# Optimization experiments

Hardware: AMD Instinct MI355X
Metric: run time of the kernel (lower is better)

## Reference

```python
import jax, jax.numpy as jnp
import numpy as np

T, B, D = 512, 16, 128   # cur_seq, batch, d_input
H = 8                    # n_heads
DH = D                   # d_head_inner = d_input in TemporalTX
P = 512                  # prev_seq = hgcn_rollout_len


def setup_inputs() -> dict:
    key = jax.random.key(0)
    ks = jax.random.split(key, 8)
    inp = {
        "inputs": jax.random.normal(ks[0], (T, B, D), jnp.float32),
        "memory": jax.random.normal(ks[1], (2, P, B, D), jnp.float32),  # n_layers+1 = 2
        "w_kv": jax.random.normal(ks[2], (2 * H * DH, D), jnp.float32) * 0.02,
        "w_q": jax.random.normal(ks[3], (H * DH, D), jnp.float32) * 0.02,
        "w_p": jax.random.normal(ks[4], (H * DH, D), jnp.float32) * 0.02,
        "w_out": jax.random.normal(ks[5], (D, H * DH), jnp.float32) * 0.02,
        "u": jax.random.normal(ks[6], (H, DH), jnp.float32) * 0.02,
        "v": jax.random.normal(ks[7], (H, DH), jnp.float32) * 0.02,
    }
    return inp


def _rel_shift(x):
    # x: [I, J, B, H] -> Transformer-XL relative shift
    I, J, b, h = x.shape
    zp = jnp.zeros((I, 1, b, h), x.dtype)
    return jnp.concatenate([zp, x], axis=1).reshape(J + 1, I, b, h)[1:].reshape(I, J, b, h)


def _pos_embs(J, d):
    # positions counting down: J-1 ... 0
    pos = jnp.arange(J - 1, -1, -1, dtype=jnp.float32)
    inv_freq = 1.0 / (10000.0 ** (jnp.arange(0.0, d, 2.0) / d))
    sin_inp = pos[:, None] * inv_freq[None, :]          # [J, d/2]
    return jnp.concatenate([jnp.sin(sin_inp), jnp.cos(sin_inp)], axis=-1)  # [J, d]


def _attention(x, mem, pe, w_kv, w_q, w_p, w_out, u, v, mask):
    cs, bs, _ = x.shape
    J = cs + mem.shape[0]
    xm = jnp.concatenate([mem, x], axis=0)              # [J, B, D]
    kv = jnp.einsum('jbe,fe->jbf', xm, w_kv)            # [J, B, 2*H*DH]
    k, vv = jnp.split(kv, 2, axis=-1)
    k = k.reshape(J, bs, H, DH)
    vv = vv.reshape(J, bs, H, DH)
    q = jnp.einsum('ibe,fe->ibf', x, w_q).reshape(cs, bs, H, DH)
    content = jnp.einsum('ibhd,jbhd->ijbh', q + u, k)   # [I, J, B, H]
    p = jnp.einsum('je,fe->jf', pe, w_p).reshape(J, H, DH)
    position = jnp.einsum('ibhd,jhd->ijbh', q + v, p)
    position = _rel_shift(position)
    attn = content + position
    attn = jnp.where(mask[:, :, None, None], -jnp.inf, attn)
    scale = 1.0 / (DH ** 0.5)
    attn = jax.nn.softmax(attn * scale, axis=1)
    out = jnp.einsum('ijbh,jbhd->ibhd', attn, vv).reshape(cs, bs, H * DH)
    return jnp.einsum('ibf,ef->ibe', out, w_out)        # [I, B, D]


def reference(inputs, memory, w_kv, w_q, w_p, w_out, u, v):
    cs, bs = inputs.shape[:2]
    mem = list(memory)                                   # unbind along layer dim
    ps = mem[0].shape[0]
    J = cs + ps
    mask = jnp.triu(jnp.ones((cs, J), bool), k=1 + ps)   # [cs, J]
    pe = _pos_embs(J, D)                                 # [J, D]
    layer_out = _attention(inputs, mem[0], pe, w_kv, w_q, w_p, w_out, u, v, mask)
    hidden = [inputs, layer_out]
    # update_memory: keep last ps entries of cat(mem, hidden), detached
    new_mem = []
    end = ps + cs
    beg = max(0, end - ps)
    for m, h in zip(mem, hidden):
        cat = jnp.concatenate([m, h], axis=0)
        new_mem.append(jax.lax.stop_gradient(cat[beg:end]))
    return layer_out, jnp.stack(new_mem)
```

## Files before the change

### kernel.cpp

```cpp
#include <hip/hip_runtime.h>


typedef short s16x8 __attribute__((ext_vector_type(8)));
typedef float f32x4 __attribute__((ext_vector_type(4)));

#define MFMA(a, b, c) __builtin_amdgcn_mfma_f32_16x16x32_bf16((a), (b), (c), 0, 0, 0)
#define LDS_FENCE() asm volatile("s_waitcnt lgkmcnt(0)" ::: "memory")

__device__ __forceinline__ unsigned short f2b(float f) {
  unsigned int x = __builtin_bit_cast(unsigned int, f);
  x += 0x7fffu + ((x >> 16) & 1u);
  return (unsigned short)(x >> 16);
}
__device__ __forceinline__ s16x8 ldg8(const unsigned short* p) {
  return *(const s16x8*)p;
}
__device__ __forceinline__ s16x8 ldf8(const float* p) {
  float4 u = ((const float4*)p)[0];
  float4 v = ((const float4*)p)[1];
  s16x8 r;
  r[0] = (short)f2b(u.x); r[1] = (short)f2b(u.y);
  r[2] = (short)f2b(u.z); r[3] = (short)f2b(u.w);
  r[4] = (short)f2b(v.x); r[5] = (short)f2b(v.y);
  r[6] = (short)f2b(v.z); r[7] = (short)f2b(v.w);
  return r;
}
__device__ __forceinline__ void gl2lds(const unsigned short* g, unsigned short* l) {
  __builtin_amdgcn_global_load_lds(
      (const __attribute__((address_space(1))) unsigned int*)(g),
      (__attribute__((address_space(3))) unsigned int*)(l), 16, 0, 0);
}

__global__ __launch_bounds__(256, 2) void k_prep(
    const float* __restrict__ wkv, const float* __restrict__ wq,
    const float* __restrict__ wp, const float* __restrict__ wout,
    unsigned short* __restrict__ wkv_b, unsigned short* __restrict__ wq_b,
    unsigned short* __restrict__ wp_b, unsigned short* __restrict__ wout_b) {
  int id = blockIdx.x * 256 + threadIdx.x;
  const float* src;
  unsigned short* dst;
  int off;
  if (id < 32768) { src = wkv; dst = wkv_b; off = id; }
  else if (id < 49152) { src = wq; dst = wq_b; off = id - 32768; }
  else if (id < 65536) { src = wp; dst = wp_b; off = id - 49152; }
  else { src = wout; dst = wout_b; off = id - 65536; }
  ((s16x8*)dst)[off] = ldf8(src + off * 8);
}

__global__ __launch_bounds__(256, 2) void k_proj(
    const float* __restrict__ x, const float* __restrict__ mem,
    const unsigned short* __restrict__ wkv_b, const unsigned short* __restrict__ wp_b,
    unsigned short* __restrict__ Kk, unsigned short* __restrict__ Vt,
    unsigned short* __restrict__ Pp) {
  __shared__ float tbuf[4][16][128];
  const int lane = threadIdx.x & 63;
  const int w = threadIdx.x >> 6;
  const int l15 = lane & 15, l4 = lane >> 4;

  if (blockIdx.x < 1024) {
    const int ncg = (blockIdx.x & 7) * 2;
    const int b = (blockIdx.x >> 3) & 15;
    const int jb = (blockIdx.x >> 7) * 128 + w * 32;

    s16x8 A[2][4];
#pragma unroll
    for (int g = 0; g < 2; ++g) {
      int jr = jb + g * 16 + l15;
      const float* arow =
          (jr < 512 ? mem + (jr * 16 + b) * 128 : x + ((jr - 512) * 16 + b) * 128) + l4 * 8;
      A[g][0] = ldf8(arow); A[g][1] = ldf8(arow + 32);
      A[g][2] = ldf8(arow + 64); A[g][3] = ldf8(arow + 96);
    }

    for (int q = 0; q < 2; ++q) {
      const int nc = ncg + q;
      f32x4 acc[2][8] = {};
#pragma unroll
      for (int fc = 0; fc < 8; ++fc) {
        const unsigned short* brow = wkv_b + (nc * 128 + fc * 16 + l15) * 128 + l4 * 8;
        s16x8 b0 = ldg8(brow), b1 = ldg8(brow + 32), b2 = ldg8(brow + 64), b3 = ldg8(brow + 96);
#pragma unroll
        for (int g = 0; g < 2; ++g) {
          acc[g][fc] = MFMA(A[g][0], b0, acc[g][fc]);
          acc[g][fc] = MFMA(A[g][1], b1, acc[g][fc]);
          acc[g][fc] = MFMA(A[g][2], b2, acc[g][fc]);
          acc[g][fc] = MFMA(A[g][3], b3, acc[g][fc]);
        }
      }

      if (nc < 8) {
#pragma unroll
        for (int g = 0; g < 2; ++g)
#pragma unroll
          for (int fc = 0; fc < 8; ++fc)
#pragma unroll
            for (int r = 0; r < 4; ++r) {
              int j = jb + g * 16 + l4 * 4 + r;
              Kk[((b * 8 + nc) * 1024 + j) * 128 + fc * 16 + l15] = f2b(acc[g][fc][r]);
            }
      } else {
        const int h = nc - 8;
#pragma unroll
        for (int g = 0; g < 2; ++g) {
          LDS_FENCE();
#pragma unroll
          for (int fc = 0; fc < 8; ++fc)
#pragma unroll
            for (int r = 0; r < 4; ++r) tbuf[w][l4 * 4 + r][fc * 16 + l15] = acc[g][fc][r];
          LDS_FENCE();
#pragma unroll
          for (int half = 0; half < 2; ++half) {
            int dd = half * 64 + lane;
            unsigned int wd[8];
#pragma unroll
            for (int pw = 0; pw < 8; ++pw) {
              unsigned int lo = f2b(tbuf[w][2 * pw][dd]);
              unsigned int hi = f2b(tbuf[w][2 * pw + 1][dd]);
              wd[pw] = lo | (hi << 16);
            }
            unsigned short* dst = Vt + ((b * 8 + h) * 128 + dd) * 1024 + jb + g * 16;
            ((uint4*)dst)[0] = make_uint4(wd[0], wd[1], wd[2], wd[3]);
            ((uint4*)dst)[1] = make_uint4(wd[4], wd[5], wd[6], wd[7]);
          }
        }
      }
    }
  } else {
    const int pidx = blockIdx.x - 1024;
    const int nc = pidx & 7;
    const int c0 = ((pidx >> 3) * 4 + w) * 16;

    const float pos = (float)(1023 - (c0 + l15));
    s16x8 a[4];
#pragma unroll
    for (int ks = 0; ks < 4; ++ks)
#pragma unroll
      for (int jj = 0; jj < 8; ++jj) {
        int e = ks * 32 + l4 * 8 + jj;
        int t = e & 63;
        float ang = pos * exp2f(-0.20762050593046014f * (float)t);
        float val = (e < 64) ? sinf(ang) : cosf(ang);
        a[ks][jj] = (short)f2b(val);
      }

    f32x4 acc[8] = {};
#pragma unroll
    for (int fc = 0; fc < 8; ++fc) {
      const unsigned short* brow = wp_b + (nc * 128 + fc * 16 + l15) * 128 + l4 * 8;
      acc[fc] = MFMA(a[0], ldg8(brow), acc[fc]);
      acc[fc] = MFMA(a[1], ldg8(brow + 32), acc[fc]);
      acc[fc] = MFMA(a[2], ldg8(brow + 64), acc[fc]);
      acc[fc] = MFMA(a[3], ldg8(brow + 96), acc[fc]);
    }
#pragma unroll
    for (int fc = 0; fc < 8; ++fc)
#pragma unroll
      for (int r = 0; r < 4; ++r)
        Pp[(nc * 1024 + c0 + l4 * 4 + r) * 128 + fc * 16 + l15] = f2b(acc[fc][r]);
  }
}

__global__ __launch_bounds__(256, 2) void k_flash(
    const float* __restrict__ x, const unsigned short* __restrict__ wq_b,
    const unsigned short* __restrict__ Kk, const unsigned short* __restrict__ Vt,
    const unsigned short* __restrict__ Pp,
    const float* __restrict__ uu, const float* __restrict__ vv,
    unsigned short* __restrict__ OA) {
  __shared__ __align__(16) unsigned short L[37376];
  unsigned short* LK = L;
  unsigned short* LV = L + 8192;
  unsigned short* LP = L + 16384;
  unsigned short* PB = L + 32768;

  const int lane = threadIdx.x & 63;
  const int w = threadIdx.x >> 6;
  const int bh = blockIdx.x & 127;
  const int igw = 7 - (blockIdx.x >> 7);
  const int iw = igw * 64 + w * 16;
  const int b = bh >> 3, h = bh & 7;
  const int l15 = lane & 15, l4 = lane >> 4;
  const int cb4 = 28 - igw * 4;
  const float CSCALE = 0.08838834764831845f * 1.4426950408889634f;

  const unsigned short* K_b = Kk + bh * (1024 * 128);
  const unsigned short* V_b = Vt + bh * (128 * 1024);
  const unsigned short* P_h = Pp + h * (1024 * 128);
  const int tmax = igw + 9;

#pragma unroll
  for (int q = 0; q < 4; ++q)
    gl2lds(K_b + (w * 16 + l15) * 128 + q * 32 + l4 * 8, LK + (w * 4 + q) * 512);
#pragma unroll
  for (int q = 0; q < 4; ++q) {
    int m = w * 4 + q, fd = m >> 1, ks = m & 1;
    gl2lds(V_b + (fd * 16 + l15) * 1024 + ks * 32 + l4 * 8, LV + m * 512);
  }

  s16x8 qu[4], qv[4];
  {
    const float* arow = x + ((iw + l15) * 16 + b) * 128 + l4 * 8;
    s16x8 a0 = ldf8(arow), a1 = ldf8(arow + 32), a2 = ldf8(arow + 64), a3 = ldf8(arow + 96);
    f32x4 qd[8] = {};
#pragma unroll
    for (int fc = 0; fc < 8; ++fc) {
      const unsigned short* brow = wq_b + (h * 128 + fc * 16 + l15) * 128 + l4 * 8;
      qd[fc] = MFMA(a0, ldg8(brow), qd[fc]);
      qd[fc] = MFMA(a1, ldg8(brow + 32), qd[fc]);
      qd[fc] = MFMA(a2, ldg8(brow + 64), qd[fc]);
      qd[fc] = MFMA(a3, ldg8(brow + 96), qd[fc]);
    }
    unsigned short* qs = LP + w * 2176;
#pragma unroll
    for (int fc = 0; fc < 8; ++fc) {
      float ud = uu[h * 128 + fc * 16 + l15];
#pragma unroll
      for (int r = 0; r < 4; ++r)
        qs[(l4 * 4 + r) * 136 + fc * 16 + l15] = f2b((qd[fc][r] + ud) * CSCALE);
    }
    LDS_FENCE();
#pragma unroll
    for (int ks = 0; ks < 4; ++ks)
      qu[ks] = *(const s16x8*)&qs[l15 * 136 + ks * 32 + l4 * 8];
    LDS_FENCE();
#pragma unroll
    for (int fc = 0; fc < 8; ++fc) {
      float vd = vv[h * 128 + fc * 16 + l15];
#pragma unroll
      for (int r = 0; r < 4; ++r)
        qs[(l4 * 4 + r) * 136 + fc * 16 + l15] = f2b((qd[fc][r] + vd) * CSCALE);
    }
    LDS_FENCE();
#pragma unroll
    for (int ks = 0; ks < 4; ++ks)
      qv[ks] = *(const s16x8*)&qs[l15 * 136 + ks * 32 + l4 * 8];
  }
  __syncthreads();

#pragma unroll
  for (int q = 0; q < 8; ++q) {
    int m = w * 8 + q, rc = m >> 2, ks = m & 3;
    int gchunk = cb4 + rc, slot = gchunk & 7;
    int grow = gchunk * 16 + l15;
    grow = (grow > 1023) ? 1023 : grow;
    gl2lds(P_h + grow * 128 + ks * 32 + l4 * 8, LP + (slot * 4 + ks) * 512);
  }
  __syncthreads();

  f32x4 O[8] = {};
  float rs[4] = {0.f, 0.f, 0.f, 0.f};

  for (int t = 0; t < tmax; ++t) {
    const int j0 = t * 64;
    const int jp = (t + 1 < tmax) ? j0 + 64 : j0;

    f32x4 sc[4];
#pragma unroll
    for (int fc = 0; fc < 4; ++fc) {
      f32x4 t4 = {};
#pragma unroll
      for (int ks = 0; ks < 4; ++ks)
        t4 = MFMA(qu[ks], *(const s16x8*)&LK[(fc * 4 + ks) * 512 + lane * 8], t4);
      sc[fc] = t4;
    }

    __syncthreads();

#pragma unroll
    for (int q = 0; q < 4; ++q)
      gl2lds(K_b + (jp + w * 16 + l15) * 128 + q * 32 + l4 * 8, LK + (w * 4 + q) * 512);

    f32x4 sp[5];
#pragma unroll
    for (int pc = 0; pc < 5; ++pc) {
      f32x4 t4 = {};
      int slot = (cb4 + 4 * t + 3 - w + pc) & 7;
#pragma unroll
      for (int ks = 0; ks < 4; ++ks)
        t4 = MFMA(qv[ks], *(const s16x8*)&LP[(slot * 4 + ks) * 512 + lane * 8], t4);
      sp[pc] = t4;
    }

    unsigned short* pb = PB + w * 1152;
#pragma unroll
    for (int fc = 0; fc < 4; ++fc)
#pragma unroll
      for (int r = 0; r < 4; ++r) {
        int li = l4 * 4 + r;
        int jj = fc * 16 + l15;
        int cc = jj - li + 15;
        int src = (lane & 48) | (cc & 15);
        float g0 = __shfl(sp[fc][r], src, 64);
        float g1 = __shfl(sp[fc + 1][r], src, 64);
        float pv = ((cc >> 4) == fc) ? g0 : g1;
        float logit = sc[fc][r] + pv;
        if (j0 + jj > iw + li + 512) logit = -60.0f;
        float p = exp2f(logit);
        rs[r] += p;
        pb[li * 72 + jj] = f2b(p);
      }

    s16x8 pa0 = *(const s16x8*)&pb[l15 * 72 + l4 * 8];
    s16x8 pa1 = *(const s16x8*)&pb[l15 * 72 + 32 + l4 * 8];
#pragma unroll
    for (int fd = 0; fd < 8; ++fd) {
      O[fd] = MFMA(pa0, *(const s16x8*)&LV[(fd * 2) * 512 + lane * 8], O[fd]);
      O[fd] = MFMA(pa1, *(const s16x8*)&LV[(fd * 2 + 1) * 512 + lane * 8], O[fd]);
    }

    __syncthreads();

#pragma unroll
    for (int q = 0; q < 4; ++q) {
      int m = w * 4 + q, fd = m >> 1, ks = m & 1;
      gl2lds(V_b + (fd * 16 + l15) * 1024 + jp + ks * 32 + l4 * 8, LV + m * 512);
    }
#pragma unroll
    for (int q = 0; q < 4; ++q) {
      int ks = q;
      int gchunk = cb4 + 4 * t + 8 + w, slot = gchunk & 7;
      int grow = gchunk * 16 + l15;
      grow = (grow > 1023) ? 1023 : grow;
      gl2lds(P_h + grow * 128 + ks * 32 + l4 * 8, LP + (slot * 4 + ks) * 512);
    }
  }

  float lrow[4];
#pragma unroll
  for (int r = 0; r < 4; ++r) {
    float s = rs[r];
#pragma unroll
    for (int off = 1; off < 16; off <<= 1) s += __shfl_xor(s, off, 64);
    lrow[r] = s;
  }
#pragma unroll
  for (int fd = 0; fd < 8; ++fd)
#pragma unroll
    for (int r = 0; r < 4; ++r) {
      int li = l4 * 4 + r;
      float o = O[fd][r] / lrow[r];
      OA[((iw + li) * 16 + b) * 1024 + h * 128 + fd * 16 + l15] = f2b(o);
    }
}

__global__ __launch_bounds__(256, 2) void k_out(
    const unsigned short* __restrict__ OA, const unsigned short* __restrict__ wout_b,
    const float* __restrict__ x, float* __restrict__ out) {
  const int lane = threadIdx.x & 63;
  const int w = threadIdx.x >> 6;
  const int qtr = blockIdx.x & 3;
  const int rt = (blockIdx.x >> 2) * 4 + w;
  const int l15 = lane & 15, l4 = lane >> 4;

  f32x4 acc[2] = {};
  const unsigned short* arow = OA + (rt * 16 + l15) * 1024 + l4 * 8;
#pragma unroll 4
  for (int ks = 0; ks < 32; ++ks) {
    s16x8 a = ldg8(arow + ks * 32);
#pragma unroll
    for (int fc = 0; fc < 2; ++fc) {
      const unsigned short* brow =
          wout_b + (qtr * 32 + fc * 16 + l15) * 1024 + ks * 32 + l4 * 8;
      acc[fc] = MFMA(a, ldg8(brow), acc[fc]);
    }
  }
#pragma unroll
  for (int fc = 0; fc < 2; ++fc)
#pragma unroll
    for (int r = 0; r < 4; ++r) {
      int rg = rt * 16 + l4 * 4 + r;
      int e = qtr * 32 + fc * 16 + l15;
      float v = acc[fc][r];
      out[rg * 128 + e] = v;
      out[2097152 + rg * 128 + e] = v;
    }
  const int gid = blockIdx.x * 4 + w;
  const float4* src = (const float4*)(x + gid * 512);
  float4* dst = (float4*)(out + 1048576 + gid * 512);
  dst[lane] = src[lane];
  dst[64 + lane] = src[64 + lane];
}

extern "C" void kernel_launch(void* const* d_in, const int* in_sizes, int n_in,
                              void* d_out, int out_size, void* d_ws, size_t ws_size,
                              hipStream_t stream) {
  (void)in_sizes; (void)n_in; (void)out_size; (void)ws_size;
  const float* x    = (const float*)d_in[0];
  const float* mem  = (const float*)d_in[1];
  const float* wkv  = (const float*)d_in[2];
  const float* wq   = (const float*)d_in[3];
  const float* wp   = (const float*)d_in[4];
  const float* wout = (const float*)d_in[5];
  const float* uu   = (const float*)d_in[6];
  const float* vv   = (const float*)d_in[7];
  float* out = (float*)d_out;
  unsigned short* ws = (unsigned short*)d_ws;

  unsigned short* Kk     = ws;
  unsigned short* Vt     = ws + 16777216;
  unsigned short* Pp     = ws + 33554432;
  unsigned short* OA     = ws + 34603008;
  unsigned short* wkv_b  = ws + 42991616;
  unsigned short* wq_b   = ws + 43253760;
  unsigned short* wp_b   = ws + 43384832;
  unsigned short* wout_b = ws + 43515904;

  k_prep<<<320, 256, 0, stream>>>(wkv, wq, wp, wout, wkv_b, wq_b, wp_b, wout_b);
  k_proj<<<1152, 256, 0, stream>>>(x, mem, wkv_b, wp_b, Kk, Vt, Pp);
  k_flash<<<1024, 256, 0, stream>>>(x, wq_b, Kk, Vt, Pp, uu, vv, OA);
  k_out<<<512, 256, 0, stream>>>(OA, wout_b, x, out);
}
```

Baseline: 259.4 us.

## Fuse weight conversion into projection kernel and vectorize K stores via LDS

Removes the separate weight-prep kernel launch: the KV and positional projections now read fp32 weights directly and convert them to bf16 in registers, and extra blocks in the projection kernel convert wq and wout for later kernels. K outputs are staged through a padded LDS tile so each lane writes contiguous 16-byte vectors instead of scattered 2-byte stores. This trades one kernel launch and a weight round-trip for twice the global weight read bytes in the projection kernel and extra LDS traffic.

Result: slower. 286.6 us (+10.5%).

```diff
diff --git a/kernel.cpp b/kernel.cpp
--- a/kernel.cpp
+++ b/kernel.cpp
@@ -31,28 +31,14 @@
       (__attribute__((address_space(3))) unsigned int*)(l), 16, 0, 0);
 }
 
-__global__ __launch_bounds__(256, 2) void k_prep(
-    const float* __restrict__ wkv, const float* __restrict__ wq,
-    const float* __restrict__ wp, const float* __restrict__ wout,
-    unsigned short* __restrict__ wkv_b, unsigned short* __restrict__ wq_b,
-    unsigned short* __restrict__ wp_b, unsigned short* __restrict__ wout_b) {
-  int id = blockIdx.x * 256 + threadIdx.x;
-  const float* src;
-  unsigned short* dst;
-  int off;
-  if (id < 32768) { src = wkv; dst = wkv_b; off = id; }
-  else if (id < 49152) { src = wq; dst = wq_b; off = id - 32768; }
-  else if (id < 65536) { src = wp; dst = wp_b; off = id - 49152; }
-  else { src = wout; dst = wout_b; off = id - 65536; }
-  ((s16x8*)dst)[off] = ldf8(src + off * 8);
-}
-
 __global__ __launch_bounds__(256, 2) void k_proj(
     const float* __restrict__ x, const float* __restrict__ mem,
-    const unsigned short* __restrict__ wkv_b, const unsigned short* __restrict__ wp_b,
+    const float* __restrict__ wkv, const float* __restrict__ wp,
+    const float* __restrict__ wq, const float* __restrict__ wout,
     unsigned short* __restrict__ Kk, unsigned short* __restrict__ Vt,
-    unsigned short* __restrict__ Pp) {
-  __shared__ float tbuf[4][16][128];
+    unsigned short* __restrict__ Pp,
+    unsigned short* __restrict__ wq_b, unsigned short* __restrict__ wout_b) {
+  __shared__ float tbuf[4][16][129];
   const int lane = threadIdx.x & 63;
   const int w = threadIdx.x >> 6;
   const int l15 = lane & 15, l4 = lane >> 4;
@@ -77,8 +63,8 @@
       f32x4 acc[2][8] = {};
 #pragma unroll
       for (int fc = 0; fc < 8; ++fc) {
-        const unsigned short* brow = wkv_b + (nc * 128 + fc * 16 + l15) * 128 + l4 * 8;
-        s16x8 b0 = ldg8(brow), b1 = ldg8(brow + 32), b2 = ldg8(brow + 64), b3 = ldg8(brow + 96);
+        const float* brow = wkv + (nc * 128 + fc * 16 + l15) * 128 + l4 * 8;
+        s16x8 b0 = ldf8(brow), b1 = ldf8(brow + 32), b2 = ldf8(brow + 64), b3 = ldf8(brow + 96);
 #pragma unroll
         for (int g = 0; g < 2; ++g) {
           acc[g][fc] = MFMA(A[g][0], b0, acc[g][fc]);
@@ -90,14 +76,26 @@
 
       if (nc < 8) {
 #pragma unroll
-        for (int g = 0; g < 2; ++g)
+        for (int g = 0; g < 2; ++g) {
+          LDS_FENCE();
 #pragma unroll
           for (int fc = 0; fc < 8; ++fc)
 #pragma unroll
-            for (int r = 0; r < 4; ++r) {
-              int j = jb + g * 16 + l4 * 4 + r;
-              Kk[((b * 8 + nc) * 1024 + j) * 128 + fc * 16 + l15] = f2b(acc[g][fc][r]);
-            }
+            for (int r = 0; r < 4; ++r) tbuf[w][l4 * 4 + r][fc * 16 + l15] = acc[g][fc][r];
+          LDS_FENCE();
+          int m = l15, c8 = l4;
+          unsigned int wd[16];
+#pragma unroll
+          for (int i = 0; i < 16; ++i) {
+            unsigned int lo = f2b(tbuf[w][m][c8 * 32 + 2 * i]);
+            unsigned int hi = f2b(tbuf[w][m][c8 * 32 + 2 * i + 1]);
+            wd[i] = lo | (hi << 16);
+          }
+          unsigned short* dst = Kk + ((b * 8 + nc) * 1024 + jb + g * 16 + m) * 128 + c8 * 32;
+#pragma unroll
+          for (int i = 0; i < 4; ++i)
+            ((uint4*)dst)[i] = make_uint4(wd[4 * i], wd[4 * i + 1], wd[4 * i + 2], wd[4 * i + 3]);
+        }
       } else {
         const int h = nc - 8;
 #pragma unroll
@@ -125,7 +123,7 @@
         }
       }
     }
-  } else {
+  } else if (blockIdx.x < 1152) {
     const int pidx = blockIdx.x - 1024;
     const int nc = pidx & 7;
     const int c0 = ((pidx >> 3) * 4 + w) * 16;
@@ -146,17 +144,21 @@
     f32x4 acc[8] = {};
 #pragma unroll
     for (int fc = 0; fc < 8; ++fc) {
-      const unsigned short* brow = wp_b + (nc * 128 + fc * 16 + l15) * 128 + l4 * 8;
-      acc[fc] = MFMA(a[0], ldg8(brow), acc[fc]);
-      acc[fc] = MFMA(a[1], ldg8(brow + 32), acc[fc]);
-      acc[fc] = MFMA(a[2], ldg8(brow + 64), acc[fc]);
-      acc[fc] = MFMA(a[3], ldg8(brow + 96), acc[fc]);
+      const float* brow = wp + (nc * 128 + fc * 16 + l15) * 128 + l4 * 8;
+      acc[fc] = MFMA(a[0], ldf8(brow), acc[fc]);
+      acc[fc] = MFMA(a[1], ldf8(brow + 32), acc[fc]);
+      acc[fc] = MFMA(a[2], ldf8(brow + 64), acc[fc]);
+      acc[fc] = MFMA(a[3], ldf8(brow + 96), acc[fc]);
     }
 #pragma unroll
     for (int fc = 0; fc < 8; ++fc)
 #pragma unroll
       for (int r = 0; r < 4; ++r)
         Pp[(nc * 1024 + c0 + l4 * 4 + r) * 128 + fc * 16 + l15] = f2b(acc[fc][r]);
+  } else {
+    int id = (blockIdx.x - 1152) * 256 + threadIdx.x;
+    if (id < 16384) ((s16x8*)wq_b)[id] = ldf8(wq + id * 8);
+    else ((s16x8*)wout_b)[id - 16384] = ldf8(wout + (id - 16384) * 8);
   }
 }
 
@@ -399,13 +401,10 @@
   unsigned short* Vt     = ws + 16777216;
   unsigned short* Pp     = ws + 33554432;
   unsigned short* OA     = ws + 34603008;
-  unsigned short* wkv_b  = ws + 42991616;
-  unsigned short* wq_b   = ws + 43253760;
-  unsigned short* wp_b   = ws + 43384832;
-  unsigned short* wout_b = ws + 43515904;
-
-  k_prep<<<320, 256, 0, stream>>>(wkv, wq, wp, wout, wkv_b, wq_b, wp_b, wout_b);
-  k_proj<<<1152, 256, 0, stream>>>(x, mem, wkv_b, wp_b, Kk, Vt, Pp);
+  unsigned short* wq_b   = ws + 42991616;
+  unsigned short* wout_b = ws + 43122688;
+
+  k_proj<<<1280, 256, 0, stream>>>(x, mem, wkv, wp, wq, wout, Kk, Vt, Pp, wq_b, wout_b);
   k_flash<<<1024, 256, 0, stream>>>(x, wq_b, Kk, Vt, Pp, uu, vv, OA);
   k_out<<<512, 256, 0, stream>>>(OA, wout_b, x, out);
 }
```
